# Optimization experiments

Hardware: AMD Instinct MI355X
Metric: run time of the kernel (lower is better)

Reference implementation:

```python
import jax, jax.numpy as jnp
import numpy as np

B, S, D, V, H, L, NM = 16, 512, 768, 30522, 12, 12, 77
HD = D // H  # 64
FF = 4 * D
EPS = 1e-5


def setup_inputs() -> dict:
    key = jax.random.key(0)
    ks = jax.random.split(key, 32)
    sc = 0.02
    n = lambda k, shp: jax.random.normal(k, shp, dtype=jnp.float32) * sc
    d = {}
    d["token_ids"] = jax.random.randint(ks[0], (B, S), 0, V)
    d["segment_ids"] = jax.random.randint(ks[1], (B, S), 0, 2)
    d["mask_ids"] = jax.random.randint(ks[2], (B, NM), 0, S)
    d["tok_emb"] = n(ks[3], (V, D))
    d["pos_emb"] = n(ks[4], (S, D))
    d["seg_emb"] = n(ks[5], (2, D))
    d["dense_w"] = n(ks[6], (V, D))
    d["dense_b"] = jnp.zeros((V,), jnp.float32)
    # per-layer params stacked on leading L axis (torch Linear convention: y = x @ W.T + b)
    d["Wq"] = n(ks[7], (L, D, D)); d["bq"] = jnp.zeros((L, D), jnp.float32)
    d["Wk"] = n(ks[8], (L, D, D)); d["bk"] = jnp.zeros((L, D), jnp.float32)
    d["Wv"] = n(ks[9], (L, D, D)); d["bv"] = jnp.zeros((L, D), jnp.float32)
    d["Wo"] = n(ks[10], (L, D, D)); d["bo"] = jnp.zeros((L, D), jnp.float32)
    d["W1"] = n(ks[11], (L, FF, D)); d["b1"] = jnp.zeros((L, FF), jnp.float32)
    d["W2"] = n(ks[12], (L, D, FF)); d["b2"] = jnp.zeros((L, D), jnp.float32)
    d["g1"] = jnp.ones((L, D), jnp.float32); d["be1"] = jnp.zeros((L, D), jnp.float32)
    d["g2"] = jnp.ones((L, D), jnp.float32); d["be2"] = jnp.zeros((L, D), jnp.float32)
    return d


def _ln(x, g, b):
    m = jnp.mean(x, -1, keepdims=True)
    v = jnp.mean(jnp.square(x - m), -1, keepdims=True)
    return (x - m) * jax.lax.rsqrt(v + EPS) * g + b


def _encoder_stack(x, layer_params):
    def layer(x, p):
        Wq, bq, Wk, bk, Wv, bv, Wo, bo, W1, b1, W2, b2, g1, be1, g2, be2 = p
        q = (x @ Wq.T + bq).reshape(B, S, H, HD).transpose(0, 2, 1, 3)  # bhsd
        k = (x @ Wk.T + bk).reshape(B, S, H, HD).transpose(0, 2, 1, 3)
        v = (x @ Wv.T + bv).reshape(B, S, H, HD).transpose(0, 2, 1, 3)
        scores = jnp.einsum('bhqd,bhkd->bhqk', q, k) / jnp.sqrt(jnp.float32(HD))
        attn = jax.nn.softmax(scores, axis=-1)
        o = jnp.einsum('bhqk,bhkd->bhqd', attn, v).transpose(0, 2, 1, 3).reshape(B, S, D)
        x = _ln(x + (o @ Wo.T + bo), g1, be1)
        h = jax.nn.gelu(x @ W1.T + b1, approximate=False)  # torch nn.GELU default is exact
        h = h @ W2.T + b2
        return _ln(x + h, g2, be2), None
    x, _ = jax.lax.scan(layer, x, layer_params)
    return x


def reference(token_ids, segment_ids, mask_ids, tok_emb, pos_emb, seg_emb,
              dense_w, dense_b, Wq, bq, Wk, bk, Wv, bv, Wo, bo,
              W1, b1, W2, b2, g1, be1, g2, be2):
    x = tok_emb[token_ids] + seg_emb[segment_ids] + pos_emb[None, :, :]  # [B,S,D]
    x = _encoder_stack(x, (Wq, bq, Wk, bk, Wv, bv, Wo, bo, W1, b1, W2, b2, g1, be1, g2, be2))
    idx = jnp.broadcast_to(mask_ids[:, :, None], (B, NM, D))
    out = jnp.take_along_axis(x, idx, axis=1)  # [B,NM,D]
    return out @ dense_w.T + dense_b  # [B,NM,V]
```

## Files before the change

kernel.cpp:

```cpp
#include <hip/hip_runtime.h>
#include <stdint.h>

typedef uint16_t u16;
typedef uint32_t u32;
typedef uint64_t u64;
typedef short short8 __attribute__((ext_vector_type(8)));
typedef float f32x4 __attribute__((ext_vector_type(4)));

#define DEV static __device__ __forceinline__

DEV u16 f2bf(float f){
  u32 x = __builtin_bit_cast(u32, f);
  return (u16)((x + 0x7fffu + ((x >> 16) & 1u)) >> 16);
}

DEV float bf2f(u16 u){
  u32 v = (u32)u << 16;
  return __builtin_bit_cast(float, v);
}

DEV f32x4 mfma16(short8 a, short8 b, f32x4 c){
  return __builtin_amdgcn_mfma_f32_16x16x32_bf16(a, b, c, 0, 0, 0);
}

DEV void async16(const void* g, void* l){
  __builtin_amdgcn_global_load_lds(
      (const __attribute__((address_space(1))) u32*)g,
      (__attribute__((address_space(3))) u32*)l, 16, 0, 0);
}

__global__ __launch_bounds__(256)
void embed_kernel(const int* __restrict__ tid, const int* __restrict__ sid,
                  const float* __restrict__ tok, const float* __restrict__ pos,
                  const float* __restrict__ seg, u16* __restrict__ xb)
{
  const int row = blockIdx.x;
  const int s = row & 511;
  const int tk = tid[row], sg = sid[row];
  const int t = threadIdx.x;
#pragma unroll
  for (int e = 0; e < 3; ++e){
    int i = t + e*256;
    float v = tok[(u64)tk*768 + i] + seg[(u64)sg*768 + i] + pos[(u64)s*768 + i];
    xb[(u64)row*768 + i] = f2bf(v);
  }
}

__global__ __launch_bounds__(256)
void cvt_bf16(const float4* __restrict__ in, ushort4* __restrict__ out, int n4)
{
  int i = blockIdx.x*256 + threadIdx.x;
  if (i >= n4) return;
  float4 f = in[i];
  ushort4 o;
  o.x = f2bf(f.x); o.y = f2bf(f.y); o.z = f2bf(f.z); o.w = f2bf(f.w);
  out[i] = o;
}

__global__ __launch_bounds__(256)
void cvt_layer(const float4* __restrict__ Wq, const float4* __restrict__ Wk,
               const float4* __restrict__ Wv, const float4* __restrict__ Wo,
               const float4* __restrict__ W1, const float4* __restrict__ W2,
               ushort4* __restrict__ wqkv, ushort4* __restrict__ wob,
               ushort4* __restrict__ w1b, ushort4* __restrict__ w2b)
{
  const int i = blockIdx.x*256 + threadIdx.x;
  const int S = 147456;
  float4 f; ushort4* dst; int di;
  if      (i <   S)       { f = Wq[i];            dst = wqkv; di = i; }
  else if (i < 2*S)       { f = Wk[i - S];        dst = wqkv; di = i; }
  else if (i < 3*S)       { f = Wv[i - 2*S];      dst = wqkv; di = i; }
  else if (i < 4*S)       { f = Wo[i - 3*S];      dst = wob;  di = i - 3*S; }
  else if (i < 4*S+589824){ f = W1[i - 4*S];      dst = w1b;  di = i - 4*S; }
  else                    { f = W2[i - 4*S-589824]; dst = w2b; di = i - 4*S - 589824; }
  ushort4 o;
  o.x = f2bf(f.x); o.y = f2bf(f.y); o.z = f2bf(f.z); o.w = f2bf(f.w);
  dst[di] = o;
}

__global__ __launch_bounds__(256)
void concat_bias(const float* __restrict__ bq, const float* __restrict__ bk,
                 const float* __restrict__ bv, float* __restrict__ out)
{
  const int l = blockIdx.x;
  const int t = threadIdx.x;
#pragma unroll
  for (int e = 0; e < 3; ++e){
    int i = t + e*256;
    out[(u64)l*2304 + i]        = bq[(u64)l*768 + i];
    out[(u64)l*2304 + 768 + i]  = bk[(u64)l*768 + i];
    out[(u64)l*2304 + 1536 + i] = bv[(u64)l*768 + i];
  }
}

DEV void stage128(const u16* __restrict__ X, int ld, int limit,
                  int rowbase, int k0, u16* lds, int t)
{
  const int rl  = t >> 2;
  const int col = (((t & 3) ^ ((t >> 3) & 3))) << 3;
  int r0 = rowbase + rl;       if (r0 > limit-1) r0 = limit-1;
  int r1 = rowbase + rl + 64;  if (r1 > limit-1) r1 = limit-1;
  async16(X + (u64)r0*ld + k0 + col, lds + t*8);
  async16(X + (u64)r1*ld + k0 + col, lds + 2048 + t*8);
}

DEV short8 ldfrag(const u16* buf, int row, int slot){
  return *(const short8*)(buf + row*32 + (slot << 3));
}

template<int EPI>
__global__ __launch_bounds__(256)
void gemm3r(const u16* __restrict__ A, const u16* __restrict__ W,
            const float* __restrict__ bias, const u16* __restrict__ xres,
            void* __restrict__ Cout, int M, int N, int K, int GM)
{
  __shared__ u16 sm[24576];
  const int t = threadIdx.x;
  const int w = t >> 6, l = t & 63;
  const int lr = l & 15, lg = l >> 4;
  const int wm = (w >> 1)*64, wn = (w & 1)*64;
  const int xr = (lr >> 1) & 3;
  const int slot = lg ^ xr;

  const int nwg = gridDim.x, orig = blockIdx.x;
  const int q = nwg >> 3, r = nwg & 7;
  const int xcd = orig & 7, sl8 = orig >> 3;
  const int wgid = (xcd < r ? xcd*(q+1) : r*(q+1) + (xcd-r)*q) + sl8;
  const int bm = wgid % GM, bn = wgid / GM;

  f32x4 acc[4][4] = {};
  short8 af[4], bf[4];

  const int NT = K >> 5;
  stage128(A, K, M, bm*128,  0, sm,          t);
  stage128(W, K, N, bn*128,  0, sm + 4096,   t);
  stage128(A, K, M, bm*128, 32, sm + 8192,   t);
  stage128(W, K, N, bn*128, 32, sm + 12288,  t);
  asm volatile("s_waitcnt vmcnt(4)" ::: "memory");
  __builtin_amdgcn_s_barrier();

  for (int tt = 0; tt < NT; ++tt){
    const int rs  = (tt % 3) * 8192;
    const int rs2 = ((tt + 2) % 3) * 8192;
    const int k2  = (tt + 2) * 32;
    const bool st2 = (tt + 2) < NT;
    const u16* Ar = sm + rs;
    const u16* Br = sm + rs + 4096;

    af[0] = ldfrag(Ar, wm + lr, slot);
    af[1] = ldfrag(Ar, wm + 16 + lr, slot);
#pragma unroll
    for (int ni = 0; ni < 4; ++ni) bf[ni] = ldfrag(Br, wn + ni*16 + lr, slot);
    if (st2) stage128(A, K, M, bm*128, k2, sm + rs2, t);
    __builtin_amdgcn_s_barrier();
    __builtin_amdgcn_s_setprio(1);
#pragma unroll
    for (int mi = 0; mi < 2; ++mi)
#pragma unroll
      for (int ni = 0; ni < 4; ++ni)
        acc[mi][ni] = mfma16(af[mi], bf[ni], acc[mi][ni]);
    __builtin_amdgcn_s_setprio(0);
    __builtin_amdgcn_s_barrier();

    af[2] = ldfrag(Ar, wm + 32 + lr, slot);
    af[3] = ldfrag(Ar, wm + 48 + lr, slot);
    if (st2) stage128(W, K, N, bn*128, k2, sm + rs2 + 4096, t);
    __builtin_amdgcn_s_barrier();
    __builtin_amdgcn_s_setprio(1);
#pragma unroll
    for (int mi = 2; mi < 4; ++mi)
#pragma unroll
      for (int ni = 0; ni < 4; ++ni)
        acc[mi][ni] = mfma16(af[mi], bf[ni], acc[mi][ni]);
    __builtin_amdgcn_s_setprio(0);
    if (st2) asm volatile("s_waitcnt vmcnt(4)" ::: "memory");
    else     asm volatile("s_waitcnt vmcnt(0)" ::: "memory");
    __builtin_amdgcn_s_barrier();
  }

  __syncthreads();
  constexpr int EPLD = 68;
  float* epw = (float*)sm + w*(16*EPLD);
#pragma unroll
  for (int mi = 0; mi < 4; ++mi){
#pragma unroll
    for (int ni = 0; ni < 4; ++ni){
      int col = bn*128 + wn + ni*16 + lr;
      float bv = bias ? bias[col < N ? col : N-1] : 0.f;
#pragma unroll
      for (int rr = 0; rr < 4; ++rr){
        float v = acc[mi][ni][rr] + bv;
        if constexpr (EPI == 2) v = 0.5f*v*(1.0f + erff(v*0.70710678118f));
        epw[(lg*4 + rr)*EPLD + ni*16 + lr] = v;
      }
    }
    asm volatile("s_waitcnt lgkmcnt(0)" ::: "memory");
    if constexpr (EPI == 0){
#pragma unroll
      for (int ps = 0; ps < 4; ++ps){
        int rloc = ps*4 + (l >> 4);
        int row = bm*128 + wm + mi*16 + rloc;
        int col = bn*128 + wn + (l & 15)*4;
        f32x4 v4 = *(const f32x4*)&epw[rloc*EPLD + (l & 15)*4];
        if (row < M){
          if (col + 3 < N){
            if (xres){
              ushort4 x4 = *(const ushort4*)(xres + (u64)row*N + col);
              v4[0] += bf2f(x4.x); v4[1] += bf2f(x4.y);
              v4[2] += bf2f(x4.z); v4[3] += bf2f(x4.w);
            }
            *(f32x4*)((float*)Cout + (u64)row*N + col) = v4;
          } else {
#pragma unroll
            for (int j = 0; j < 4; ++j)
              if (col + j < N){
                float vv = v4[j];
                if (xres) vv += bf2f(xres[(u64)row*N + col + j]);
                ((float*)Cout)[(u64)row*N + col + j] = vv;
              }
          }
        }
      }
    } else {
#pragma unroll
      for (int ps = 0; ps < 2; ++ps){
        int rloc = ps*8 + (l >> 3);
        int row = bm*128 + wm + mi*16 + rloc;
        int col = bn*128 + wn + (l & 7)*8;
        f32x4 a4 = *(const f32x4*)&epw[rloc*EPLD + (l & 7)*8];
        f32x4 b4 = *(const f32x4*)&epw[rloc*EPLD + (l & 7)*8 + 4];
        short8 o8;
        o8[0] = f2bf(a4[0]); o8[1] = f2bf(a4[1]); o8[2] = f2bf(a4[2]); o8[3] = f2bf(a4[3]);
        o8[4] = f2bf(b4[0]); o8[5] = f2bf(b4[1]); o8[6] = f2bf(b4[2]); o8[7] = f2bf(b4[3]);
        if (row < M){
          if (col + 7 < N) *(short8*)((u16*)Cout + (u64)row*N + col) = o8;
          else {
#pragma unroll
            for (int j = 0; j < 8; ++j)
              if (col + j < N) ((u16*)Cout)[(u64)row*N + col + j] = (u16)o8[j];
          }
        }
      }
    }
    asm volatile("s_waitcnt lgkmcnt(0)" ::: "memory");
  }
}

DEV void stage_tile(const u16* __restrict__ X, int ld, int limit,
                    int rowbase, int k0, u16* lds, int t)
{
  const int rl  = t >> 2;
  const int col = (((t & 3) ^ ((t >> 3) & 3))) << 3;
  int r0 = rowbase + rl;        if (r0 > limit-1) r0 = limit-1;
  int r1 = rowbase + rl + 128;  if (r1 > limit-1) r1 = limit-1;
  async16(X + (u64)r0*ld + k0 + col, lds + t*8);
  async16(X + (u64)r1*ld + k0 + col, lds + 4096 + t*8);
}

__global__ __launch_bounds__(512)
void gemm8v(const u16* __restrict__ A, const u16* __restrict__ W,
            const float* __restrict__ bias, float* __restrict__ Cout,
            int M, int N, int K, int GM)
{
  __shared__ u16 sm[49152];
  u16* Ab = sm;
  u16* Bb = sm + 24576;
  const int t = threadIdx.x;
  const int w = t >> 6, l = t & 63;
  const int lr = l & 15, lg = l >> 4;
  const int wr = w >> 2, wc = w & 3;
  const int xr = (lr >> 1) & 3;
  const int slot = lg ^ xr;

  const int nwg = gridDim.x, orig = blockIdx.x;
  const int q = nwg >> 3, r = nwg & 7;
  const int xcd = orig & 7, sl8 = orig >> 3;
  const int wgid = (xcd < r ? xcd*(q+1) : r*(q+1) + (xcd-r)*q) + sl8;
  const int bm = wgid % GM, bn = wgid / GM;

  f32x4 acc[8][4] = {};
  short8 afr[4], bfr[4];

  const int NT = K >> 5;
  stage_tile(A, K, M, bm*256,  0, Ab,        t);
  stage_tile(W, K, N, bn*256,  0, Bb,        t);
  stage_tile(A, K, M, bm*256, 32, Ab + 8192, t);
  stage_tile(W, K, N, bn*256, 32, Bb + 8192, t);
  asm volatile("s_waitcnt vmcnt(4)" ::: "memory");
  __builtin_amdgcn_s_barrier();

  for (int tt = 0; tt < NT; ++tt){
    const int rs = (tt % 3) * 8192;
    const int rs2 = ((tt + 2) % 3) * 8192;
    const int k2 = (tt + 2)*32;
    const u16* Ar = Ab + rs;
    const u16* Br = Bb + rs;
#pragma unroll
    for (int mi = 0; mi < 4; ++mi) afr[mi] = ldfrag(Ar, wr*128 + mi*16 + lr, slot);
#pragma unroll
    for (int ni = 0; ni < 4; ++ni) bfr[ni] = ldfrag(Br, wc*64 + ni*16 + lr, slot);
    if (tt + 2 < NT) stage_tile(A, K, M, bm*256, k2, Ab + rs2, t);
    __builtin_amdgcn_s_barrier();
    __builtin_amdgcn_s_setprio(1);
#pragma unroll
    for (int mi = 0; mi < 4; ++mi)
#pragma unroll
      for (int ni = 0; ni < 4; ++ni)
        acc[mi][ni] = mfma16(afr[mi], bfr[ni], acc[mi][ni]);
    __builtin_amdgcn_s_setprio(0);
    __builtin_amdgcn_s_barrier();
#pragma unroll
    for (int mi = 0; mi < 4; ++mi) afr[mi] = ldfrag(Ar, wr*128 + (mi+4)*16 + lr, slot);
    if (tt + 2 < NT) stage_tile(W, K, N, bn*256, k2, Bb + rs2, t);
    __builtin_amdgcn_s_barrier();
    __builtin_amdgcn_s_setprio(1);
#pragma unroll
    for (int mi = 0; mi < 4; ++mi)
#pragma unroll
      for (int ni = 0; ni < 4; ++ni)
        acc[mi+4][ni] = mfma16(afr[mi], bfr[ni], acc[mi+4][ni]);
    __builtin_amdgcn_s_setprio(0);
    if (tt + 2 < NT) asm volatile("s_waitcnt vmcnt(4)" ::: "memory");
    else             asm volatile("s_waitcnt vmcnt(0)" ::: "memory");
    __builtin_amdgcn_s_barrier();
  }

  __syncthreads();
  constexpr int EPLD = 68;
  float* epw = (float*)sm + w*(16*EPLD);
  const int growbase = bm*256 + wr*128;
  const int gcolbase = bn*256 + wc*64;
#pragma unroll
  for (int mi = 0; mi < 8; ++mi){
#pragma unroll
    for (int ni = 0; ni < 4; ++ni){
      int col = gcolbase + ni*16 + lr;
      float bv = bias ? bias[col < N ? col : N-1] : 0.f;
#pragma unroll
      for (int rr = 0; rr < 4; ++rr)
        epw[(lg*4 + rr)*EPLD + ni*16 + lr] = acc[mi][ni][rr] + bv;
    }
    asm volatile("s_waitcnt lgkmcnt(0)" ::: "memory");
#pragma unroll
    for (int ps = 0; ps < 4; ++ps){
      int rloc = ps*4 + (l >> 4);
      int row = growbase + mi*16 + rloc;
      int col = gcolbase + (l & 15)*4;
      f32x4 v4 = *(const f32x4*)&epw[rloc*EPLD + (l & 15)*4];
      if (row < M){
        if (col + 3 < N) *(f32x4*)(Cout + (u64)row*N + col) = v4;
        else {
#pragma unroll
          for (int j = 0; j < 4; ++j)
            if (col + j < N) Cout[(u64)row*N + col + j] = v4[j];
        }
      }
    }
    asm volatile("s_waitcnt lgkmcnt(0)" ::: "memory");
  }
}

__global__ __launch_bounds__(256)
void transpose_v(const u16* __restrict__ qkv, u16* __restrict__ vt)
{
  __shared__ u16 tile[64][72];
  const int st = blockIdx.x, h = blockIdx.y, b = blockIdx.z;
  const int t = threadIdx.x;
#pragma unroll
  for (int e = 0; e < 2; ++e){
    int lin = t + e*256;
    int s = lin >> 3, c8 = (lin & 7)*8;
    *(short8*)(&tile[s][c8]) =
        *(const short8*)(qkv + (u64)(b*512 + st*64 + s)*2304 + 1536 + h*64 + c8);
  }
  __syncthreads();
#pragma unroll
  for (int e = 0; e < 2; ++e){
    int lin = t + e*256;
    int d = lin >> 3, s8 = (lin & 7)*8;
    short8 ov;
#pragma unroll
    for (int i = 0; i < 8; ++i) ov[i] = (short)tile[s8 + i][d];
    *(short8*)(vt + ((u64)(b*12 + h)*64 + d)*512 + st*64 + s8) = ov;
  }
}

__global__ __launch_bounds__(256)
void attn_kernel(const u16* __restrict__ qkv, const u16* __restrict__ vt,
                 u16* __restrict__ ob)
{
  __shared__ u16 p_lds[4][16][72];
  const int t = threadIdx.x, w = t >> 6, ll = t & 63;
  const int lr = ll & 15, lg = ll >> 4;
  const int qt = blockIdx.x, h = blockIdx.y, b = blockIdx.z;
  const int q0 = qt*64 + w*16;
  const float C = 0.125f * 1.44269504f;

  const u16* qrow = qkv + (u64)(b*512 + q0 + lr)*2304 + h*64 + 8*lg;
  const short8 qf0 = *(const short8*)qrow;
  const short8 qf1 = *(const short8*)(qrow + 32);

  const u16* kbh = qkv + (u64)(b*512)*2304 + 768 + h*64;
  const u16* vth = vt + (u64)(b*12 + h)*64*512;

  f32x4 lacc = {0.f, 0.f, 0.f, 0.f};
  f32x4 o_acc[4] = {};

  for (int jt = 0; jt < 8; ++jt){
    const int jb = jt*64;
    f32x4 s[4] = {};
#pragma unroll
    for (int jn = 0; jn < 4; ++jn){
      const u16* kr = kbh + (u64)(jb + jn*16 + lr)*2304 + 8*lg;
      short8 kf0 = *(const short8*)kr;
      short8 kf1 = *(const short8*)(kr + 32);
      s[jn] = mfma16(qf0, kf0, s[jn]);
      s[jn] = mfma16(qf1, kf1, s[jn]);
    }
#pragma unroll
    for (int jn = 0; jn < 4; ++jn)
#pragma unroll
      for (int r = 0; r < 4; ++r){
        float pv = exp2f(s[jn][r]*C);
        s[jn][r] = pv;
        lacc[r] += pv;
      }
#pragma unroll
    for (int jn = 0; jn < 4; ++jn)
#pragma unroll
      for (int r = 0; r < 4; ++r)
        p_lds[w][4*lg + r][jn*16 + lr] = f2bf(s[jn][r]);
    asm volatile("s_waitcnt lgkmcnt(0)" ::: "memory");
    short8 pa0 = *(const short8*)(&p_lds[w][lr][8*lg]);
    short8 pa1 = *(const short8*)(&p_lds[w][lr][32 + 8*lg]);
#pragma unroll
    for (int nd = 0; nd < 4; ++nd){
      const u16* vr = vth + (u64)(nd*16 + lr)*512 + jb + 8*lg;
      short8 vf0 = *(const short8*)vr;
      short8 vf1 = *(const short8*)(vr + 32);
      o_acc[nd] = mfma16(pa0, vf0, o_acc[nd]);
      o_acc[nd] = mfma16(pa1, vf1, o_acc[nd]);
    }
    asm volatile("s_waitcnt lgkmcnt(0)" ::: "memory");
  }
  float l_r[4];
#pragma unroll
  for (int r = 0; r < 4; ++r){
    float v = lacc[r];
#pragma unroll
    for (int m = 1; m < 16; m <<= 1) v += __shfl_xor(v, m);
    l_r[r] = 1.f / v;
  }
#pragma unroll
  for (int nd = 0; nd < 4; ++nd)
#pragma unroll
    for (int r = 0; r < 4; ++r)
      p_lds[w][4*lg + r][nd*16 + lr] = f2bf(o_acc[nd][r]*l_r[r]);
  asm volatile("s_waitcnt lgkmcnt(0)" ::: "memory");
#pragma unroll
  for (int ps = 0; ps < 2; ++ps){
    int row = ps*8 + (ll >> 3);
    short8 ov = *(const short8*)(&p_lds[w][row][(ll & 7)*8]);
    *(short8*)(ob + (u64)(b*512 + q0 + row)*768 + h*64 + (ll & 7)*8) = ov;
  }
}

__global__ __launch_bounds__(256)
void ln_only(const float* __restrict__ yin,
             const float* __restrict__ g, const float* __restrict__ be,
             u16* __restrict__ xbout)
{
  __shared__ float sred[8];
  const int row = blockIdx.x, t = threadIdx.x;
  const int w = t >> 6, ll = t & 63;
  float v[3]; float s = 0.f, sq = 0.f;
#pragma unroll
  for (int e = 0; e < 3; ++e){
    int i = t + e*256;
    float val = yin[(u64)row*768 + i];
    v[e] = val; s += val; sq += val*val;
  }
#pragma unroll
  for (int m = 1; m < 64; m <<= 1){ s += __shfl_xor(s, m); sq += __shfl_xor(sq, m); }
  if (ll == 0){ sred[w] = s; sred[4 + w] = sq; }
  __syncthreads();
  s  = sred[0] + sred[1] + sred[2] + sred[3];
  sq = sred[4] + sred[5] + sred[6] + sred[7];
  const float mean = s*(1.f/768.f);
  const float rstd = rsqrtf(sq*(1.f/768.f) - mean*mean + 1e-5f);
#pragma unroll
  for (int e = 0; e < 3; ++e){
    int i = t + e*256;
    xbout[(u64)row*768 + i] = f2bf((v[e] - mean)*rstd*g[i] + be[i]);
  }
}

__global__ __launch_bounds__(256)
void gather_rows(const u16* __restrict__ xb, const int* __restrict__ mids,
                 u16* __restrict__ xg)
{
  const int row = blockIdx.x;
  const int b = row / 77;
  const int src = b*512 + mids[row];
  const int t = threadIdx.x;
#pragma unroll
  for (int e = 0; e < 3; ++e){
    int i = t + e*256;
    xg[(u64)row*768 + i] = xb[(u64)src*768 + i];
  }
}

extern "C" void kernel_launch(void* const* d_in, const int* in_sizes, int n_in,
                              void* d_out, int out_size, void* d_ws, size_t ws_size,
                              hipStream_t stream)
{
  const int*   token_ids  = (const int*)  d_in[0];
  const int*   segment_ids= (const int*)  d_in[1];
  const int*   mask_ids   = (const int*)  d_in[2];
  const float* tok_emb    = (const float*)d_in[3];
  const float* pos_emb    = (const float*)d_in[4];
  const float* seg_emb    = (const float*)d_in[5];
  const float* dense_w    = (const float*)d_in[6];
  const float* dense_b    = (const float*)d_in[7];
  const float* Wq = (const float*)d_in[8];  const float* bq = (const float*)d_in[9];
  const float* Wk = (const float*)d_in[10]; const float* bk = (const float*)d_in[11];
  const float* Wv = (const float*)d_in[12]; const float* bv = (const float*)d_in[13];
  const float* Wo = (const float*)d_in[14]; const float* bo = (const float*)d_in[15];
  const float* W1 = (const float*)d_in[16]; const float* b1 = (const float*)d_in[17];
  const float* W2 = (const float*)d_in[18]; const float* b2 = (const float*)d_in[19];
  const float* g1 = (const float*)d_in[20]; const float* be1= (const float*)d_in[21];
  const float* g2 = (const float*)d_in[22]; const float* be2= (const float*)d_in[23];

  char* p = (char*)d_ws;
  auto alloc = [&](size_t bytes)->char*{
    char* r = p; p += (bytes + 255) & ~(size_t)255; return r;
  };
  const u64 T = 8192;
  float* y    = (float*)alloc(T*768*4);
  u16*   xb   = (u16*)  alloc(T*768*2);
  u16*   qkvb = (u16*)  alloc(T*2304*2);
  u16*   vT   = (u16*)  alloc(T*768*2);
  u16*   obuf = (u16*)  alloc(T*768*2);
  u16*   h1b  = (u16*)  alloc(T*3072*2);
  u16*   xg   = (u16*)  alloc((u64)1232*768*2);
  u16*   wqkv = (u16*)  alloc((u64)2304*768*2);
  u16*   wob  = (u16*)  alloc((u64)768*768*2);
  u16*   w1b  = (u16*)  alloc((u64)3072*768*2);
  u16*   w2b  = (u16*)  alloc((u64)3072*768*2);
  float* bqkv = (float*)alloc((u64)12*2304*4);
  u16*   dwb  = h1b;

  if ((size_t)(p - (char*)d_ws) > ws_size) return;

  embed_kernel<<<dim3(8192), dim3(256), 0, stream>>>(
      token_ids, segment_ids, tok_emb, pos_emb, seg_emb, xb);
  concat_bias<<<dim3(12), dim3(256), 0, stream>>>(bq, bk, bv, bqkv);

  for (int l = 0; l < 12; ++l){
    cvt_layer<<<dim3(6912), dim3(256), 0, stream>>>(
        (const float4*)(Wq + (u64)l*589824), (const float4*)(Wk + (u64)l*589824),
        (const float4*)(Wv + (u64)l*589824), (const float4*)(Wo + (u64)l*589824),
        (const float4*)(W1 + (u64)l*2359296), (const float4*)(W2 + (u64)l*2359296),
        (ushort4*)wqkv, (ushort4*)wob, (ushort4*)w1b, (ushort4*)w2b);

    gemm3r<1><<<dim3(64*18), dim3(256), 0, stream>>>(xb, wqkv, bqkv + (u64)l*2304, nullptr,
                                                     qkvb, 8192, 2304, 768, 64);

    transpose_v<<<dim3(8, 12, 16), dim3(256), 0, stream>>>(qkvb, vT);
    attn_kernel<<<dim3(8, 12, 16), dim3(256), 0, stream>>>(qkvb, vT, obuf);

    gemm3r<0><<<dim3(64*6), dim3(256), 0, stream>>>(obuf, wob, bo + (u64)l*768, xb,
                                                    y, 8192, 768, 768, 64);
    ln_only<<<dim3(8192), dim3(256), 0, stream>>>(y, g1 + (u64)l*768, be1 + (u64)l*768, xb);

    gemm3r<2><<<dim3(64*24), dim3(256), 0, stream>>>(xb, w1b, b1 + (u64)l*3072, nullptr,
                                                     h1b, 8192, 3072, 768, 64);
    gemm3r<0><<<dim3(64*6), dim3(256), 0, stream>>>(h1b, w2b, b2 + (u64)l*768, xb,
                                                    y, 8192, 768, 3072, 64);
    ln_only<<<dim3(8192), dim3(256), 0, stream>>>(y, g2 + (u64)l*768, be2 + (u64)l*768, xb);
  }

  gather_rows<<<dim3(1232), dim3(256), 0, stream>>>(xb, mask_ids, xg);
  cvt_bf16<<<dim3(22892), dim3(256), 0, stream>>>((const float4*)dense_w, (ushort4*)dwb, 5860224);
  gemm8v<<<dim3(5*120), dim3(512), 0, stream>>>(xg, dwb, dense_b, (float*)d_out,
                                                1232, 30522, 768, 5);
}
```

Before: 4.205 ms.

## Fuse V transpose into QKV GEMM epilogue and widen attention query tiles

The QKV GEMM epilogue now writes V tiles directly in transposed layout through LDS, so the separate transpose kernel and its extra global read/write pass are removed. Blocks covering V columns skip writing V to the qkv buffer. The attention kernel processes 32 query rows per wave instead of 16, reusing each loaded K and V fragment for two query tiles and halving redundant global loads. In exchange, the attention grid halves and per-thread register use rises, which may reduce occupancy.

```diff
diff --git a/kernel.cpp b/kernel.cpp
--- a/kernel.cpp
+++ b/kernel.cpp
@@ -112,7 +112,8 @@
 __global__ __launch_bounds__(256)
 void gemm3r(const u16* __restrict__ A, const u16* __restrict__ W,
             const float* __restrict__ bias, const u16* __restrict__ xres,
-            void* __restrict__ Cout, int M, int N, int K, int GM)
+            u16* __restrict__ vt, void* __restrict__ Cout,
+            int M, int N, int K, int GM)
 {
   __shared__ u16 sm[24576];
   const int t = threadIdx.x;
@@ -179,6 +180,36 @@
   }
 
   __syncthreads();
+
+  if constexpr (EPI == 1){
+    if (vt && bn*128 + wn >= 1536){
+      u16* vbuf = sm + w*4736;
+#pragma unroll
+      for (int mi = 0; mi < 4; ++mi)
+#pragma unroll
+        for (int ni = 0; ni < 4; ++ni){
+          int col = bn*128 + wn + ni*16 + lr;
+          float bv = bias ? bias[col] : 0.f;
+#pragma unroll
+          for (int rr = 0; rr < 4; ++rr)
+            vbuf[(mi*16 + lg*4 + rr)*74 + ni*16 + lr] = f2bf(acc[mi][ni][rr] + bv);
+        }
+      asm volatile("s_waitcnt lgkmcnt(0)" ::: "memory");
+      const int row0w = bm*128 + wm;
+      const int b_ = row0w >> 9, s0 = row0w & 511;
+      const int h_ = (bn*128 + wn - 1536) >> 6;
+#pragma unroll
+      for (int e = 0; e < 8; ++e){
+        int d = e*8 + (l >> 3), s8 = (l & 7)*8;
+        short8 ov;
+#pragma unroll
+        for (int i = 0; i < 8; ++i) ov[i] = (short)vbuf[(s8 + i)*74 + d];
+        *(short8*)(vt + ((u64)(b_*12 + h_)*64 + d)*512 + s0 + s8) = ov;
+      }
+      return;
+    }
+  }
+
   constexpr int EPLD = 68;
   float* epw = (float*)sm + w*(16*EPLD);
 #pragma unroll
@@ -361,104 +392,94 @@
 }
 
 __global__ __launch_bounds__(256)
-void transpose_v(const u16* __restrict__ qkv, u16* __restrict__ vt)
-{
-  __shared__ u16 tile[64][72];
-  const int st = blockIdx.x, h = blockIdx.y, b = blockIdx.z;
-  const int t = threadIdx.x;
-#pragma unroll
-  for (int e = 0; e < 2; ++e){
-    int lin = t + e*256;
-    int s = lin >> 3, c8 = (lin & 7)*8;
-    *(short8*)(&tile[s][c8]) =
-        *(const short8*)(qkv + (u64)(b*512 + st*64 + s)*2304 + 1536 + h*64 + c8);
-  }
-  __syncthreads();
-#pragma unroll
-  for (int e = 0; e < 2; ++e){
-    int lin = t + e*256;
-    int d = lin >> 3, s8 = (lin & 7)*8;
-    short8 ov;
-#pragma unroll
-    for (int i = 0; i < 8; ++i) ov[i] = (short)tile[s8 + i][d];
-    *(short8*)(vt + ((u64)(b*12 + h)*64 + d)*512 + st*64 + s8) = ov;
-  }
-}
-
-__global__ __launch_bounds__(256)
 void attn_kernel(const u16* __restrict__ qkv, const u16* __restrict__ vt,
                  u16* __restrict__ ob)
 {
-  __shared__ u16 p_lds[4][16][72];
+  __shared__ u16 p_lds[4][32][72];
   const int t = threadIdx.x, w = t >> 6, ll = t & 63;
   const int lr = ll & 15, lg = ll >> 4;
   const int qt = blockIdx.x, h = blockIdx.y, b = blockIdx.z;
-  const int q0 = qt*64 + w*16;
+  const int q0 = qt*128 + w*32;
   const float C = 0.125f * 1.44269504f;
 
-  const u16* qrow = qkv + (u64)(b*512 + q0 + lr)*2304 + h*64 + 8*lg;
-  const short8 qf0 = *(const short8*)qrow;
-  const short8 qf1 = *(const short8*)(qrow + 32);
+  short8 qf[2][2];
+#pragma unroll
+  for (int f = 0; f < 2; ++f){
+    const u16* qrow = qkv + (u64)(b*512 + q0 + f*16 + lr)*2304 + h*64 + 8*lg;
+    qf[f][0] = *(const short8*)qrow;
+    qf[f][1] = *(const short8*)(qrow + 32);
+  }
 
   const u16* kbh = qkv + (u64)(b*512)*2304 + 768 + h*64;
   const u16* vth = vt + (u64)(b*12 + h)*64*512;
 
-  f32x4 lacc = {0.f, 0.f, 0.f, 0.f};
-  f32x4 o_acc[4] = {};
+  f32x4 lacc[2] = {};
+  f32x4 o_acc[2][4] = {};
 
   for (int jt = 0; jt < 8; ++jt){
     const int jb = jt*64;
-    f32x4 s[4] = {};
+    f32x4 s[2][4] = {};
 #pragma unroll
     for (int jn = 0; jn < 4; ++jn){
       const u16* kr = kbh + (u64)(jb + jn*16 + lr)*2304 + 8*lg;
       short8 kf0 = *(const short8*)kr;
       short8 kf1 = *(const short8*)(kr + 32);
-      s[jn] = mfma16(qf0, kf0, s[jn]);
-      s[jn] = mfma16(qf1, kf1, s[jn]);
-    }
-#pragma unroll
-    for (int jn = 0; jn < 4; ++jn)
-#pragma unroll
-      for (int r = 0; r < 4; ++r){
-        float pv = exp2f(s[jn][r]*C);
-        s[jn][r] = pv;
-        lacc[r] += pv;
+#pragma unroll
+      for (int f = 0; f < 2; ++f){
+        s[f][jn] = mfma16(qf[f][0], kf0, s[f][jn]);
+        s[f][jn] = mfma16(qf[f][1], kf1, s[f][jn]);
       }
-#pragma unroll
-    for (int jn = 0; jn < 4; ++jn)
-#pragma unroll
-      for (int r = 0; r < 4; ++r)
-        p_lds[w][4*lg + r][jn*16 + lr] = f2bf(s[jn][r]);
+    }
+#pragma unroll
+    for (int f = 0; f < 2; ++f)
+#pragma unroll
+      for (int jn = 0; jn < 4; ++jn)
+#pragma unroll
+        for (int r = 0; r < 4; ++r){
+          float pv = exp2f(s[f][jn][r]*C);
+          lacc[f][r] += pv;
+          p_lds[w][f*16 + 4*lg + r][jn*16 + lr] = f2bf(pv);
+        }
     asm volatile("s_waitcnt lgkmcnt(0)" ::: "memory");
-    short8 pa0 = *(const short8*)(&p_lds[w][lr][8*lg]);
-    short8 pa1 = *(const short8*)(&p_lds[w][lr][32 + 8*lg]);
+    short8 pa[2][2];
+#pragma unroll
+    for (int f = 0; f < 2; ++f){
+      pa[f][0] = *(const short8*)(&p_lds[w][f*16 + lr][8*lg]);
+      pa[f][1] = *(const short8*)(&p_lds[w][f*16 + lr][32 + 8*lg]);
+    }
 #pragma unroll
     for (int nd = 0; nd < 4; ++nd){
       const u16* vr = vth + (u64)(nd*16 + lr)*512 + jb + 8*lg;
       short8 vf0 = *(const short8*)vr;
       short8 vf1 = *(const short8*)(vr + 32);
-      o_acc[nd] = mfma16(pa0, vf0, o_acc[nd]);
-      o_acc[nd] = mfma16(pa1, vf1, o_acc[nd]);
+#pragma unroll
+      for (int f = 0; f < 2; ++f){
+        o_acc[f][nd] = mfma16(pa[f][0], vf0, o_acc[f][nd]);
+        o_acc[f][nd] = mfma16(pa[f][1], vf1, o_acc[f][nd]);
+      }
     }
     asm volatile("s_waitcnt lgkmcnt(0)" ::: "memory");
   }
-  float l_r[4];
-#pragma unroll
-  for (int r = 0; r < 4; ++r){
-    float v = lacc[r];
-#pragma unroll
-    for (int m = 1; m < 16; m <<= 1) v += __shfl_xor(v, m);
-    l_r[r] = 1.f / v;
-  }
-#pragma unroll
-  for (int nd = 0; nd < 4; ++nd)
-#pragma unroll
-    for (int r = 0; r < 4; ++r)
-      p_lds[w][4*lg + r][nd*16 + lr] = f2bf(o_acc[nd][r]*l_r[r]);
+  float l_r[2][4];
+#pragma unroll
+  for (int f = 0; f < 2; ++f)
+#pragma unroll
+    for (int r = 0; r < 4; ++r){
+      float v = lacc[f][r];
+#pragma unroll
+      for (int m = 1; m < 16; m <<= 1) v += __shfl_xor(v, m);
+      l_r[f][r] = 1.f / v;
+    }
+#pragma unroll
+  for (int f = 0; f < 2; ++f)
+#pragma unroll
+    for (int nd = 0; nd < 4; ++nd)
+#pragma unroll
+      for (int r = 0; r < 4; ++r)
+        p_lds[w][f*16 + 4*lg + r][nd*16 + lr] = f2bf(o_acc[f][nd][r]*l_r[f][r]);
   asm volatile("s_waitcnt lgkmcnt(0)" ::: "memory");
 #pragma unroll
-  for (int ps = 0; ps < 2; ++ps){
+  for (int ps = 0; ps < 4; ++ps){
     int row = ps*8 + (ll >> 3);
     short8 ov = *(const short8*)(&p_lds[w][row][(ll & 7)*8]);
     *(short8*)(ob + (u64)(b*512 + q0 + row)*768 + h*64 + (ll & 7)*8) = ov;
@@ -564,19 +585,18 @@
         (ushort4*)wqkv, (ushort4*)wob, (ushort4*)w1b, (ushort4*)w2b);
 
     gemm3r<1><<<dim3(64*18), dim3(256), 0, stream>>>(xb, wqkv, bqkv + (u64)l*2304, nullptr,
-                                                     qkvb, 8192, 2304, 768, 64);
-
-    transpose_v<<<dim3(8, 12, 16), dim3(256), 0, stream>>>(qkvb, vT);
-    attn_kernel<<<dim3(8, 12, 16), dim3(256), 0, stream>>>(qkvb, vT, obuf);
+                                                     vT, qkvb, 8192, 2304, 768, 64);
+
+    attn_kernel<<<dim3(4, 12, 16), dim3(256), 0, stream>>>(qkvb, vT, obuf);
 
     gemm3r<0><<<dim3(64*6), dim3(256), 0, stream>>>(obuf, wob, bo + (u64)l*768, xb,
-                                                    y, 8192, 768, 768, 64);
+                                                    nullptr, y, 8192, 768, 768, 64);
     ln_only<<<dim3(8192), dim3(256), 0, stream>>>(y, g1 + (u64)l*768, be1 + (u64)l*768, xb);
 
     gemm3r<2><<<dim3(64*24), dim3(256), 0, stream>>>(xb, w1b, b1 + (u64)l*3072, nullptr,
-                                                     h1b, 8192, 3072, 768, 64);
+                                                     nullptr, h1b, 8192, 3072, 768, 64);
     gemm3r<0><<<dim3(64*6), dim3(256), 0, stream>>>(h1b, w2b, b2 + (u64)l*768, xb,
-                                                    y, 8192, 768, 3072, 64);
+                                                    nullptr, y, 8192, 768, 3072, 64);
     ln_only<<<dim3(8192), dim3(256), 0, stream>>>(y, g2 + (u64)l*768, be2 + (u64)l*768, xb);
   }
 
```

Measured after the change: 3.673 ms, median of 2. 1.15x faster.
